# Performance work log

Measured on AMD Instinct MI355X. Metric: run time of the kernel, lower is better.

## Reference

```python
import jax, jax.numpy as jnp
import numpy as np

# Tiny fixed contraction dims: M=3^(r_1-k), K=3^k, N=3^(r_2-k) with r_1=r_2=2, k=1
M, K, N = 3, 3, 3
R_O = 2  # output tensor rank -> output trailing shape (3,)*R_O == (3,3)


def setup_inputs() -> dict:
    key = jax.random.key(0)
    k1, k2 = jax.random.split(key)
    P, B, C = 4, 8192, 128
    T1 = jax.random.normal(k1, (P, B, C, M, K), dtype=jnp.float32)
    T2 = jax.random.normal(k2, (1, B, C, K, N), dtype=jnp.float32)
    return {"T1": T1, "T2": T2}


def reference(T1, T2):
    P, B, C = T1.shape[:3]
    T1m = T1.reshape(P, B, C, M, K)
    # T2 has a broadcast path dim of size 1; drop it and broadcast via einsum
    T2m = T2.reshape(B, C, K, N)
    out = jnp.einsum('pbcik,bckj->pbcij', T1m, T2m)
    return out.reshape((P, B, C) + (3,) * R_O)
```

## Files before the change

### kernel.cpp

```cpp
#include <hip/hip_runtime.h>


typedef float floatx4 __attribute__((ext_vector_type(4)));

__global__ __launch_bounds__(256) void tc33_kernel(const float* __restrict__ T1,
                                                   const float* __restrict__ T2,
                                                   float* __restrict__ out) {
    __shared__ float so[9216];
    const long long PER_P = 9LL * 8192 * 128;
    const int tid = threadIdx.x;
    const long long blockBase = (long long)blockIdx.x * 9216;
    const long long base = blockBase + tid * 36;

    float b[36];
    {
        const float4* B4 = reinterpret_cast<const float4*>(T2 + base);
        #pragma unroll
        for (int j = 0; j < 9; ++j) {
            float4 v = B4[j];
            b[4*j+0] = v.x; b[4*j+1] = v.y; b[4*j+2] = v.z; b[4*j+3] = v.w;
        }
    }

    #pragma unroll
    for (int p = 0; p < 4; ++p) {
        float a[36];
        {
            const float4* A4 = reinterpret_cast<const float4*>(T1 + p * PER_P + base);
            #pragma unroll
            for (int j = 0; j < 9; ++j) {
                float4 v = A4[j];
                a[4*j+0] = v.x; a[4*j+1] = v.y; a[4*j+2] = v.z; a[4*j+3] = v.w;
            }
        }

        float o[36];
        #pragma unroll
        for (int u = 0; u < 4; ++u) {
            #pragma unroll
            for (int i = 0; i < 3; ++i) {
                #pragma unroll
                for (int j = 0; j < 3; ++j) {
                    float s = a[u*9 + i*3 + 0] * b[u*9 + 0*3 + j];
                    s = fmaf(a[u*9 + i*3 + 1], b[u*9 + 1*3 + j], s);
                    s = fmaf(a[u*9 + i*3 + 2], b[u*9 + 2*3 + j], s);
                    o[u*9 + i*3 + j] = s;
                }
            }
        }

        if (p) __syncthreads();
        {
            floatx4* S4w = reinterpret_cast<floatx4*>(&so[tid * 36]);
            #pragma unroll
            for (int j = 0; j < 9; ++j) {
                floatx4 v;
                v.x = o[4*j+0]; v.y = o[4*j+1]; v.z = o[4*j+2]; v.w = o[4*j+3];
                S4w[j] = v;
            }
        }
        __syncthreads();

        {
            const floatx4* S4 = reinterpret_cast<const floatx4*>(so);
            floatx4* O4 = reinterpret_cast<floatx4*>(out + p * PER_P + blockBase);
            #pragma unroll
            for (int j = 0; j < 9; ++j) {
                floatx4 v = S4[tid + 256 * j];
                __builtin_nontemporal_store(v, &O4[tid + 256 * j]);
            }
        }
    }
}

extern "C" void kernel_launch(void* const* d_in, const int* in_sizes, int n_in,
                              void* d_out, int out_size, void* d_ws, size_t ws_size,
                              hipStream_t stream) {
    const float* T1 = (const float*)d_in[0];
    const float* T2 = (const float*)d_in[1];
    float* out = (float*)d_out;

    const int threads = 256;
    const int blocks = (8192 * 128 / 4) / threads;
    tc33_kernel<<<blocks, threads, 0, stream>>>(T1, T2, out);
}
```

Measured before the change: 286.5 us.

## Stage inputs through shared memory with coalesced loads, one matrix per thread

Each thread now handles one 3x3 product instead of four. Both operands are loaded with fully coalesced float4 reads into shared memory, replacing the strided per-thread 144-byte loads. Outputs are staged back through shared memory for coalesced nontemporal stores. The next P slice of T1 is prefetched into registers before the stores, and the grid grows 4x with a much smaller shared-memory footprint. The cost is more barriers per block and strided 9-float LDS accesses that may hit bank conflicts.

```diff
diff --git a/kernel.cpp b/kernel.cpp
--- a/kernel.cpp
+++ b/kernel.cpp
@@ -6,70 +6,83 @@
 __global__ __launch_bounds__(256) void tc33_kernel(const float* __restrict__ T1,
                                                    const float* __restrict__ T2,
                                                    float* __restrict__ out) {
-    __shared__ float so[9216];
+    __shared__ float sA[2304];
+    __shared__ float sB[2304];
     const long long PER_P = 9LL * 8192 * 128;
     const int tid = threadIdx.x;
-    const long long blockBase = (long long)blockIdx.x * 9216;
-    const long long base = blockBase + tid * 36;
+    const long long base = (long long)blockIdx.x * 2304;
 
-    float b[36];
+    floatx4* SA4 = reinterpret_cast<floatx4*>(sA);
+    floatx4* SB4 = reinterpret_cast<floatx4*>(sB);
+
     {
-        const float4* B4 = reinterpret_cast<const float4*>(T2 + base);
-        #pragma unroll
-        for (int j = 0; j < 9; ++j) {
-            float4 v = B4[j];
-            b[4*j+0] = v.x; b[4*j+1] = v.y; b[4*j+2] = v.z; b[4*j+3] = v.w;
+        const floatx4* Bg = reinterpret_cast<const floatx4*>(T2 + base);
+        const floatx4* Ag = reinterpret_cast<const floatx4*>(T1 + base);
+        floatx4 rb0 = Bg[tid], rb1 = Bg[tid + 256];
+        floatx4 ra0 = Ag[tid], ra1 = Ag[tid + 256];
+        SB4[tid] = rb0; SB4[tid + 256] = rb1;
+        SA4[tid] = ra0; SA4[tid + 256] = ra1;
+        if (tid < 64) {
+            floatx4 rb2 = Bg[tid + 512];
+            floatx4 ra2 = Ag[tid + 512];
+            SB4[tid + 512] = rb2;
+            SA4[tid + 512] = ra2;
         }
     }
+    __syncthreads();
+
+    float b[9];
+    #pragma unroll
+    for (int i = 0; i < 9; ++i) b[i] = sB[tid * 9 + i];
 
     #pragma unroll
     for (int p = 0; p < 4; ++p) {
-        float a[36];
-        {
-            const float4* A4 = reinterpret_cast<const float4*>(T1 + p * PER_P + base);
+        float a[9];
+        #pragma unroll
+        for (int i = 0; i < 9; ++i) a[i] = sA[tid * 9 + i];
+
+        float o[9];
+        #pragma unroll
+        for (int i = 0; i < 3; ++i) {
             #pragma unroll
-            for (int j = 0; j < 9; ++j) {
-                float4 v = A4[j];
-                a[4*j+0] = v.x; a[4*j+1] = v.y; a[4*j+2] = v.z; a[4*j+3] = v.w;
+            for (int j = 0; j < 3; ++j) {
+                float s = a[i * 3 + 0] * b[0 * 3 + j];
+                s = fmaf(a[i * 3 + 1], b[1 * 3 + j], s);
+                s = fmaf(a[i * 3 + 2], b[2 * 3 + j], s);
+                o[i * 3 + j] = s;
             }
         }
 
-        float o[36];
         #pragma unroll
-        for (int u = 0; u < 4; ++u) {
-            #pragma unroll
-            for (int i = 0; i < 3; ++i) {
-                #pragma unroll
-                for (int j = 0; j < 3; ++j) {
-                    float s = a[u*9 + i*3 + 0] * b[u*9 + 0*3 + j];
-                    s = fmaf(a[u*9 + i*3 + 1], b[u*9 + 1*3 + j], s);
-                    s = fmaf(a[u*9 + i*3 + 2], b[u*9 + 2*3 + j], s);
-                    o[u*9 + i*3 + j] = s;
-                }
-            }
+        for (int i = 0; i < 9; ++i) sB[tid * 9 + i] = o[i];
+
+        __syncthreads();
+
+        floatx4 na0, na1, na2;
+        if (p < 3) {
+            const floatx4* An =
+                reinterpret_cast<const floatx4*>(T1 + (p + 1) * PER_P + base);
+            na0 = An[tid];
+            na1 = An[tid + 256];
+            if (tid < 64) na2 = An[tid + 512];
         }
 
-        if (p) __syncthreads();
         {
-            floatx4* S4w = reinterpret_cast<floatx4*>(&so[tid * 36]);
-            #pragma unroll
-            for (int j = 0; j < 9; ++j) {
-                floatx4 v;
-                v.x = o[4*j+0]; v.y = o[4*j+1]; v.z = o[4*j+2]; v.w = o[4*j+3];
-                S4w[j] = v;
-            }
+            floatx4* O4 = reinterpret_cast<floatx4*>(out + p * PER_P + base);
+            const floatx4* S4 = reinterpret_cast<const floatx4*>(sB);
+            __builtin_nontemporal_store(S4[tid      ], &O4[tid      ]);
+            __builtin_nontemporal_store(S4[tid + 256], &O4[tid + 256]);
+            if (tid < 64)
+                __builtin_nontemporal_store(S4[tid + 512], &O4[tid + 512]);
         }
+
+        if (p < 3) {
+            SA4[tid      ] = na0;
+            SA4[tid + 256] = na1;
+            if (tid < 64) SA4[tid + 512] = na2;
+        }
+
         __syncthreads();
-
-        {
-            const floatx4* S4 = reinterpret_cast<const floatx4*>(so);
-            floatx4* O4 = reinterpret_cast<floatx4*>(out + p * PER_P + blockBase);
-            #pragma unroll
-            for (int j = 0; j < 9; ++j) {
-                floatx4 v = S4[tid + 256 * j];
-                __builtin_nontemporal_store(v, &O4[tid + 256 * j]);
-            }
-        }
     }
 }
 
@@ -81,6 +94,6 @@
     float* out = (float*)d_out;
 
     const int threads = 256;
-    const int blocks = (8192 * 128 / 4) / threads;
+    const int blocks = (8192 * 128) / 256;
     tc33_kernel<<<blocks, threads, 0, stream>>>(T1, T2, out);
 }
```

After: 285.3 us. About the same (-0.4%).
